# Kernel optimization log

Measured on AMD Instinct MI355X. Metric: run time of the kernel, lower is better.

The kernel has to match this reference:

```python
import jax, jax.numpy as jnp
import numpy as np

VOCAB = 50257
NSAMPLES = 1048576


def setup_inputs() -> dict:
    key = jax.random.key(0)
    k1, k2 = jax.random.split(key)
    # positive sampling weights (need not be normalized, as in WeightedRandomSampler)
    frequencies = jax.random.uniform(k1, (VOCAB,), dtype=jnp.float32) + 1e-3
    # pre-drawn uniforms, one per sample (replacement=True => iid draws)
    u = jax.random.uniform(k2, (NSAMPLES,), dtype=jnp.float32)
    return {"frequencies": frequencies, "u": u}


def reference(frequencies, u):
    # WeightedRandomSampler with replacement == multinomial sampling proportional
    # to frequencies. Implemented as inverse-CDF: normalize, cumsum, binary search.
    cdf = jnp.cumsum(frequencies)          # [V], unnormalized CDF
    total = cdf[-1]
    # scale uniforms into [0, total) instead of dividing the whole CDF (fewer ops)
    idx = jnp.searchsorted(cdf, u * total, side="right")  # [N] int indices
    idx = jnp.clip(idx, 0, frequencies.shape[0] - 1)
    # original returns a FloatTensor of the sampled indices
    return idx.astype(jnp.float32)
```

## Files before the change

kernel.cpp:

```cpp
#include <hip/hip_runtime.h>
#include <math.h>


#define GRP 16
#define TPB 512
#define SPT 4
#define GPT_MAX 16

__device__ __forceinline__ int physIdx(int i) { return i + (i >> 5); }

__global__ __launch_bounds__(256) void gsum_kernel(const float* __restrict__ freq,
                                                   int V, float* __restrict__ gsum) {
    const int i4 = blockIdx.x * 256 + threadIdx.x;
    const int nf4 = (V + 3) >> 2;
    float s = 0.f;
    if (i4 < nf4) {
        const int base = i4 * 4;
        if (base + 3 < V) {
            const float4 v = *reinterpret_cast<const float4*>(freq + base);
            s = v.x + v.y + v.z + v.w;
        } else {
            for (int j = 0; j < 4; ++j)
                if (base + j < V) s += freq[base + j];
        }
    }
    s += __shfl_xor(s, 1);
    s += __shfl_xor(s, 2);
    const int g = i4 >> 2;
    const int G = (V + GRP - 1) / GRP;
    if ((threadIdx.x & 3) == 0 && g < G) gsum[g] = s;
}

template <int PAD>
__global__ __launch_bounds__(TPB) void sample_kernel(const float* __restrict__ freq,
                                                     const float* __restrict__ u,
                                                     const float* __restrict__ gsum,
                                                     float* __restrict__ out,
                                                     int N, int V, int G) {
    __shared__ float sS[PAD + (PAD >> 5)];
    __shared__ float wsum[TPB / 64];
    const int t = threadIdx.x;
    const int lane = t & 63;
    const int w = t >> 6;
    const int GPT = (G + TPB - 1) / TPB;

    const int gid = blockIdx.x * TPB + t;
    const long long i0 = (long long)gid * SPT;
    float uk[SPT];
    const bool full = (i0 + SPT <= N);
    if (full) {
        const float4 A = *reinterpret_cast<const float4*>(u + i0);
        uk[0] = A.x; uk[1] = A.y; uk[2] = A.z; uk[3] = A.w;
    } else {
#pragma unroll
        for (int s = 0; s < SPT; ++s) uk[s] = (i0 + s < N) ? u[i0 + s] : 0.f;
    }

    const int g0 = t * GPT;
    float ls[GPT_MAX];
    float runv = 0.f;
#pragma unroll
    for (int k = 0; k < GPT_MAX; ++k) {
        float s = 0.f;
        if (k < GPT) { const int g = g0 + k; if (g < G) s = gsum[g]; }
        runv += s;
        ls[k] = runv;
    }
    float sc = runv;
#pragma unroll
    for (int off = 1; off <= 32; off <<= 1) {
        const float v = __shfl_up(sc, off);
        if (lane >= off) sc += v;
    }
    if (lane == 63) wsum[w] = sc;
    __syncthreads();
    float tbase = sc - runv;
    for (int k = 0; k < w; ++k) tbase += wsum[k];

#pragma unroll
    for (int k = 0; k < GPT_MAX; ++k) {
        if (k < GPT) { const int g = g0 + k; if (g < G) sS[physIdx(g)] = tbase + ls[k]; }
    }
    for (int i = G + t; i < PAD; i += TPB) sS[physIdx(i)] = INFINITY;
    __syncthreads();

    if (i0 >= N) return;

    const float total = sS[physIdx(G - 1)];

    float ok[SPT];
#pragma unroll
    for (int s = 0; s < SPT; ++s) {
        const float key = uk[s] * total;

        int pos = -1;
#pragma unroll
        for (int step = PAD >> 1; step >= 1; step >>= 1) {
            const int j = pos + step;
            pos += (sS[physIdx(j)] <= key) ? step : 0;
        }
        int g = pos + 1;
        g = (g > G - 1) ? (G - 1) : g;
        const float base = (g > 0) ? sS[physIdx(g - 1)] : 0.f;
        const int eb = g * GRP;

        float r = base;
        int cnt = 0;
        if (eb + GRP <= V) {
            const float4* fp = reinterpret_cast<const float4*>(freq + eb);
            const float4 a = fp[0], b = fp[1], c = fp[2], d = fp[3];
            r += a.x; cnt += (r <= key); r += a.y; cnt += (r <= key);
            r += a.z; cnt += (r <= key); r += a.w; cnt += (r <= key);
            r += b.x; cnt += (r <= key); r += b.y; cnt += (r <= key);
            r += b.z; cnt += (r <= key); r += b.w; cnt += (r <= key);
            r += c.x; cnt += (r <= key); r += c.y; cnt += (r <= key);
            r += c.z; cnt += (r <= key); r += c.w; cnt += (r <= key);
            r += d.x; cnt += (r <= key); r += d.y; cnt += (r <= key);
            r += d.z; cnt += (r <= key); r += d.w; cnt += (r <= key);
        } else {
            for (int j = 0; j < GRP; ++j) {
                const int idx = eb + j;
                if (idx < V) { r += freq[idx]; cnt += (r <= key); }
            }
        }
        int ans = eb + cnt;
        ans = (ans > V - 1) ? (V - 1) : ans;
        ok[s] = (float)ans;
    }

    if (full) {
        *reinterpret_cast<float4*>(out + i0) = make_float4(ok[0], ok[1], ok[2], ok[3]);
    } else {
        for (int s = 0; s < SPT; ++s)
            if (i0 + s < N) out[i0 + s] = ok[s];
    }
}

extern "C" void kernel_launch(void* const* d_in, const int* in_sizes, int n_in,
                              void* d_out, int out_size, void* d_ws, size_t ws_size,
                              hipStream_t stream) {
    const float* freq = (const float*)d_in[0];
    const float* u    = (const float*)d_in[1];
    float* out        = (float*)d_out;
    const int V = in_sizes[0];
    const int N = in_sizes[1];
    const int G = (V + GRP - 1) / GRP;

    float* gsum = (float*)d_ws;

    const int nf4 = (V + 3) >> 2;
    hipLaunchKernelGGL(gsum_kernel, dim3((nf4 + 255) / 256), dim3(256), 0, stream,
                       freq, V, gsum);

    const int NB = (N + TPB * SPT - 1) / (TPB * SPT);
    if (G < 1024) {
        hipLaunchKernelGGL(sample_kernel<1024>, dim3(NB), dim3(TPB), 0, stream,
                           freq, u, gsum, out, N, V, G);
    } else if (G < 2048) {
        hipLaunchKernelGGL(sample_kernel<2048>, dim3(NB), dim3(TPB), 0, stream,
                           freq, u, gsum, out, N, V, G);
    } else if (G < 4096) {
        hipLaunchKernelGGL(sample_kernel<4096>, dim3(NB), dim3(TPB), 0, stream,
                           freq, u, gsum, out, N, V, G);
    } else {
        hipLaunchKernelGGL(sample_kernel<8192>, dim3(NB), dim3(TPB), 0, stream,
                           freq, u, gsum, out, N, V, G);
    }
}
```

Before: 19.83 us.

## Shrink CDF groups to 4 elements and stage group sums through LDS

Group size drops from 16 to 4, so the shared-memory group CDF grows to about 12.5K entries (the PAD=16384 variant) and each sample's final global scan reads one float4 instead of four. Group sums are first copied into LDS with vectorized loads before the per-thread prefix scan, replacing strided global reads. The cost is a bigger per-block prefix build, roughly 64KB of LDS per block (lower occupancy), and a few more binary-search steps. It aims to cut per-sample global memory traffic in the final scan.

Measured after the change: 22.58 us. +13.9%, slower.

```diff
diff --git a/kernel.cpp b/kernel.cpp
--- a/kernel.cpp
+++ b/kernel.cpp
@@ -2,33 +2,27 @@
 #include <math.h>
 
 
-#define GRP 16
+#define GRP 4
 #define TPB 512
 #define SPT 4
-#define GPT_MAX 16
 
 __device__ __forceinline__ int physIdx(int i) { return i + (i >> 5); }
 
 __global__ __launch_bounds__(256) void gsum_kernel(const float* __restrict__ freq,
                                                    int V, float* __restrict__ gsum) {
-    const int i4 = blockIdx.x * 256 + threadIdx.x;
-    const int nf4 = (V + 3) >> 2;
+    const int g = blockIdx.x * 256 + threadIdx.x;
+    const int G = (V + 3) >> 2;
+    if (g >= G) return;
+    const int base = g * 4;
     float s = 0.f;
-    if (i4 < nf4) {
-        const int base = i4 * 4;
-        if (base + 3 < V) {
-            const float4 v = *reinterpret_cast<const float4*>(freq + base);
-            s = v.x + v.y + v.z + v.w;
-        } else {
-            for (int j = 0; j < 4; ++j)
-                if (base + j < V) s += freq[base + j];
-        }
+    if (base + 3 < V) {
+        const float4 v = *reinterpret_cast<const float4*>(freq + base);
+        s = v.x + v.y + v.z + v.w;
+    } else {
+        for (int j = 0; j < 4; ++j)
+            if (base + j < V) s += freq[base + j];
     }
-    s += __shfl_xor(s, 1);
-    s += __shfl_xor(s, 2);
-    const int g = i4 >> 2;
-    const int G = (V + GRP - 1) / GRP;
-    if ((threadIdx.x & 3) == 0 && g < G) gsum[g] = s;
+    gsum[g] = s;
 }
 
 template <int PAD>
@@ -37,6 +31,7 @@
                                                      const float* __restrict__ gsum,
                                                      float* __restrict__ out,
                                                      int N, int V, int G) {
+    constexpr int GPTM = PAD / TPB;
     __shared__ float sS[PAD + (PAD >> 5)];
     __shared__ float wsum[TPB / 64];
     const int t = threadIdx.x;
@@ -56,13 +51,20 @@
         for (int s = 0; s < SPT; ++s) uk[s] = (i0 + s < N) ? u[i0 + s] : 0.f;
     }
 
+    const int G4 = G >> 2;
+    const float4* gs4 = reinterpret_cast<const float4*>(gsum);
+    float4* sS4 = reinterpret_cast<float4*>(sS);
+    for (int i = t; i < G4; i += TPB) sS4[i] = gs4[i];
+    for (int i = (G4 << 2) + t; i < G; i += TPB) sS[i] = gsum[i];
+    __syncthreads();
+
     const int g0 = t * GPT;
-    float ls[GPT_MAX];
+    float ls[GPTM];
     float runv = 0.f;
 #pragma unroll
-    for (int k = 0; k < GPT_MAX; ++k) {
+    for (int k = 0; k < GPTM; ++k) {
         float s = 0.f;
-        if (k < GPT) { const int g = g0 + k; if (g < G) s = gsum[g]; }
+        if (k < GPT) { const int g = g0 + k; if (g < G) s = sS[g]; }
         runv += s;
         ls[k] = runv;
     }
@@ -78,7 +80,7 @@
     for (int k = 0; k < w; ++k) tbase += wsum[k];
 
 #pragma unroll
-    for (int k = 0; k < GPT_MAX; ++k) {
+    for (int k = 0; k < GPTM; ++k) {
         if (k < GPT) { const int g = g0 + k; if (g < G) sS[physIdx(g)] = tbase + ls[k]; }
     }
     for (int i = G + t; i < PAD; i += TPB) sS[physIdx(i)] = INFINITY;
@@ -102,23 +104,18 @@
         int g = pos + 1;
         g = (g > G - 1) ? (G - 1) : g;
         const float base = (g > 0) ? sS[physIdx(g - 1)] : 0.f;
-        const int eb = g * GRP;
+        const int eb = g << 2;
 
         float r = base;
         int cnt = 0;
-        if (eb + GRP <= V) {
-            const float4* fp = reinterpret_cast<const float4*>(freq + eb);
-            const float4 a = fp[0], b = fp[1], c = fp[2], d = fp[3];
-            r += a.x; cnt += (r <= key); r += a.y; cnt += (r <= key);
-            r += a.z; cnt += (r <= key); r += a.w; cnt += (r <= key);
-            r += b.x; cnt += (r <= key); r += b.y; cnt += (r <= key);
-            r += b.z; cnt += (r <= key); r += b.w; cnt += (r <= key);
-            r += c.x; cnt += (r <= key); r += c.y; cnt += (r <= key);
-            r += c.z; cnt += (r <= key); r += c.w; cnt += (r <= key);
-            r += d.x; cnt += (r <= key); r += d.y; cnt += (r <= key);
-            r += d.z; cnt += (r <= key); r += d.w; cnt += (r <= key);
+        if (eb + 4 <= V) {
+            const float4 f = *reinterpret_cast<const float4*>(freq + eb);
+            r += f.x; cnt += (r <= key);
+            r += f.y; cnt += (r <= key);
+            r += f.z; cnt += (r <= key);
+            r += f.w; cnt += (r <= key);
         } else {
-            for (int j = 0; j < GRP; ++j) {
+            for (int j = 0; j < 4; ++j) {
                 const int idx = eb + j;
                 if (idx < V) { r += freq[idx]; cnt += (r <= key); }
             }
@@ -148,22 +145,21 @@
 
     float* gsum = (float*)d_ws;
 
-    const int nf4 = (V + 3) >> 2;
-    hipLaunchKernelGGL(gsum_kernel, dim3((nf4 + 255) / 256), dim3(256), 0, stream,
+    hipLaunchKernelGGL(gsum_kernel, dim3((G + 255) / 256), dim3(256), 0, stream,
                        freq, V, gsum);
 
     const int NB = (N + TPB * SPT - 1) / (TPB * SPT);
-    if (G < 1024) {
-        hipLaunchKernelGGL(sample_kernel<1024>, dim3(NB), dim3(TPB), 0, stream,
-                           freq, u, gsum, out, N, V, G);
-    } else if (G < 2048) {
+    if (G < 2048) {
         hipLaunchKernelGGL(sample_kernel<2048>, dim3(NB), dim3(TPB), 0, stream,
                            freq, u, gsum, out, N, V, G);
     } else if (G < 4096) {
         hipLaunchKernelGGL(sample_kernel<4096>, dim3(NB), dim3(TPB), 0, stream,
                            freq, u, gsum, out, N, V, G);
+    } else if (G < 8192) {
+        hipLaunchKernelGGL(sample_kernel<8192>, dim3(NB), dim3(TPB), 0, stream,
+                           freq, u, gsum, out, N, V, G);
     } else {
-        hipLaunchKernelGGL(sample_kernel<8192>, dim3(NB), dim3(TPB), 0, stream,
+        hipLaunchKernelGGL(sample_kernel<16384>, dim3(NB), dim3(TPB), 0, stream,
                            freq, u, gsum, out, N, V, G);
     }
 }
```
